# Kernel optimization log

Hardware: AMD Instinct MI355X
Metric: run time of the kernel (lower is better)

## Reference

```python
import jax, jax.numpy as jnp
import numpy as np

FEATS = 1024
HEAD = 16
MLP_HIDDEN = 4096
HEAD_DIM = FEATS // HEAD
SQRT_D = float(FEATS) ** 0.5  # module scales by sqrt(feats), not sqrt(head_dim)
LN_EPS = 1e-5


def layer_norm(x, g, b):
    mu = jnp.mean(x, axis=-1, keepdims=True)
    var = jnp.mean(jnp.square(x - mu), axis=-1, keepdims=True)
    return (x - mu) * jax.lax.rsqrt(var + LN_EPS) * g + b


def setup_inputs() -> dict:
    key = jax.random.key(0)
    ks = jax.random.split(key, 12)
    s = 1.0 / np.sqrt(FEATS)
    s2 = 1.0 / np.sqrt(MLP_HIDDEN)
    return {
        "x": jax.random.normal(ks[0], (2, 2048, FEATS), dtype=jnp.float32),
        "ln1_g": jnp.ones((FEATS,), jnp.float32),
        "ln1_b": jnp.zeros((FEATS,), jnp.float32),
        "wq": jax.random.normal(ks[1], (FEATS, FEATS), jnp.float32) * s,
        "bq": jnp.zeros((FEATS,), jnp.float32),
        "wk": jax.random.normal(ks[2], (FEATS, FEATS), jnp.float32) * s,
        "bk": jnp.zeros((FEATS,), jnp.float32),
        "wv": jax.random.normal(ks[3], (FEATS, FEATS), jnp.float32) * s,
        "bv": jnp.zeros((FEATS,), jnp.float32),
        "wo": jax.random.normal(ks[4], (FEATS, FEATS), jnp.float32) * s,
        "bo": jnp.zeros((FEATS,), jnp.float32),
        "ln2_g": jnp.ones((FEATS,), jnp.float32),
        "ln2_b": jnp.zeros((FEATS,), jnp.float32),
        "w1": jax.random.normal(ks[5], (MLP_HIDDEN, FEATS), jnp.float32) * s,
        "b1": jnp.zeros((MLP_HIDDEN,), jnp.float32),
        "w2": jax.random.normal(ks[6], (FEATS, MLP_HIDDEN), jnp.float32) * s2,
        "b2": jnp.zeros((FEATS,), jnp.float32),
    }


def reference(x, ln1_g, ln1_b, wq, bq, wk, bk, wv, bv, wo, bo,
              ln2_g, ln2_b, w1, b1, w2, b2):
    b, n, f = x.shape
    h = layer_norm(x, ln1_g, ln1_b)
    # qkv projections (torch Linear: y = x @ W.T + b)
    q = (h @ wq.T + bq).reshape(b, n, HEAD, HEAD_DIM).transpose(0, 2, 1, 3)
    k = (h @ wk.T + bk).reshape(b, n, HEAD, HEAD_DIM).transpose(0, 2, 1, 3)
    v = (h @ wv.T + bv).reshape(b, n, HEAD, HEAD_DIM).transpose(0, 2, 1, 3)
    score = jax.nn.softmax(jnp.einsum('bhif,bhjf->bhij', q, k) / SQRT_D, axis=-1)
    attn = jnp.einsum('bhij,bhjf->bihf', score, v).reshape(b, n, f)
    o = attn @ wo.T + bo
    out1 = o + x
    h2 = layer_norm(out1, ln2_g, ln2_b)
    mlp = jax.nn.relu(jax.nn.relu(h2 @ w1.T + b1) @ w2.T + b2)
    return mlp + out1
```

## Files before the change

kernel.cpp:

```cpp
#include <hip/hip_runtime.h>
#include <hip/hip_bf16.h>

#define FEATS 1024
#define NH 16
#define HD 64
#define SEQ 2048
#define BATCH 2
#define MTOT (BATCH*SEQ)
#define MLPH 4096
#define QSCALE 0.04508422277369218f

typedef __attribute__((ext_vector_type(8))) short bf16x8;
typedef __attribute__((ext_vector_type(4))) short bf16x4;
typedef __attribute__((ext_vector_type(4))) float f32x4;

static_assert(sizeof(bf16x8) == 16, "bf16x8 must be 16B");

__device__ __forceinline__ unsigned short f2bf(float f) {
    unsigned int u = __float_as_uint(f);
    unsigned int lsb = (u >> 16) & 1u;
    u += 0x7fffu + lsb;
    return (unsigned short)(u >> 16);
}

#define ASYNC16(GP, LP) __builtin_amdgcn_global_load_lds( \
    (const __attribute__((address_space(1))) void*)(GP),  \
    (__attribute__((address_space(3))) void*)(LP), 16, 0, 0)

__global__ __launch_bounds__(256) void cvt_all_kernel(
    const float* __restrict__ wq, const float* __restrict__ wk,
    const float* __restrict__ wv, const float* __restrict__ wo,
    const float* __restrict__ w1, const float* __restrict__ w2,
    unsigned short* __restrict__ dst) {
    const size_t i = ((size_t)blockIdx.x * 256 + threadIdx.x) * 4;
    const size_t MB = (size_t)1024 * 1024;
    const float* s;
    size_t off;
    float sc = 1.0f;
    if (i < MB)            { s = wq; off = i;          sc = QSCALE; }
    else if (i < 2 * MB)   { s = wk; off = i - MB; }
    else if (i < 3 * MB)   { s = wv; off = i - 2 * MB; }
    else if (i < 4 * MB)   { s = wo; off = i - 3 * MB; }
    else if (i < 8 * MB)   { s = w1; off = i - 4 * MB; }
    else                   { s = w2; off = i - 8 * MB; }
    float4 v = *(const float4*)(s + off);
    ushort4 o;
    o.x = f2bf(v.x * sc); o.y = f2bf(v.y * sc);
    o.z = f2bf(v.z * sc); o.w = f2bf(v.w * sc);
    *(ushort4*)(dst + i) = o;
}

__global__ __launch_bounds__(256) void concat3_kernel(const float* __restrict__ a,
                                                      const float* __restrict__ b,
                                                      const float* __restrict__ c,
                                                      float* __restrict__ o) {
    int i = blockIdx.x * 256 + threadIdx.x;
    float v = (i < 1024) ? a[i] * QSCALE : ((i < 2048) ? b[i - 1024] : c[i - 2048]);
    o[i] = v;
}

__global__ __launch_bounds__(256) void ln_kernel(const float* __restrict__ x,
                                                 const float* __restrict__ g,
                                                 const float* __restrict__ bta,
                                                 unsigned short* __restrict__ h) {
    __shared__ float red[8];
    const int row = blockIdx.x;
    const int t = threadIdx.x;
    const float* xr = x + (size_t)row * FEATS;
    float4 v = ((const float4*)xr)[t];
    float s  = v.x + v.y + v.z + v.w;
    float ss = v.x * v.x + v.y * v.y + v.z * v.z + v.w * v.w;
#pragma unroll
    for (int off = 1; off < 64; off <<= 1) {
        s  += __shfl_xor(s, off);
        ss += __shfl_xor(ss, off);
    }
    const int w = t >> 6;
    if ((t & 63) == 0) { red[w] = s; red[4 + w] = ss; }
    __syncthreads();
    s  = red[0] + red[1] + red[2] + red[3];
    ss = red[4] + red[5] + red[6] + red[7];
    const float mu  = s * (1.f / FEATS);
    const float var = ss * (1.f / FEATS) - mu * mu;
    const float rs  = rsqrtf(var + 1e-5f);
    float4 gv = ((const float4*)g)[t];
    float4 bv = ((const float4*)bta)[t];
    ushort4 ov;
    ov.x = f2bf((v.x - mu) * rs * gv.x + bv.x);
    ov.y = f2bf((v.y - mu) * rs * gv.y + bv.y);
    ov.z = f2bf((v.z - mu) * rs * gv.z + bv.z);
    ov.w = f2bf((v.w - mu) * rs * gv.w + bv.w);
    ((ushort4*)h)[(size_t)row * (FEATS / 4) + t] = ov;
}

template <bool RELU, bool ADD, bool OUTBF16>
__global__ __launch_bounds__(256, 3)
void gemm_kernel(const unsigned short* __restrict__ A,
                 const unsigned short* __restrict__ W,
                 const float* __restrict__ bias,
                 const float* __restrict__ addend,
                 void* __restrict__ outp,
                 int M, int N, int K, int gx) {
    __shared__ unsigned short lds[3][2][128 * 32];

    const int t = threadIdx.x;
    const int w = t >> 6, lane = t & 63;
    const int wr = w >> 1, wc = w & 1;
    const int li = lane & 15, lj = lane >> 4;

    const int nwg = gridDim.x;
    const int cpx = nwg >> 3;
    const int wg = blockIdx.x;
    const int swz = (wg & 7) * cpx + (wg >> 3);
    const int mb = (swz / gx) * 128, nb = (swz % gx) * 128;

    const int srow = lane >> 2;
    const int scg = ((lane & 3) ^ (srow & 3)) * 8;
    const unsigned short* gA = A + (size_t)(mb + w * 16 + srow) * K + scg;
    const unsigned short* gB = W + (size_t)(nb + w * 16 + srow) * K + scg;
    const size_t half = (size_t)64 * K;
    const int lbase = w * 512 + lane * 8;

    const int rsw = (lj ^ (li & 3)) * 8;

    const int nt = K >> 5;

#define STAGE(BUF, K0)                                             \
    do {                                                           \
        unsigned short* la_ = &lds[BUF][0][lbase];                 \
        unsigned short* lb_ = &lds[BUF][1][lbase];                 \
        ASYNC16(gA + (K0), la_);                                   \
        ASYNC16(gA + half + (K0), la_ + 2048);                     \
        ASYNC16(gB + (K0), lb_);                                   \
        ASYNC16(gB + half + (K0), lb_ + 2048);                     \
    } while (0)

    STAGE(0, 0);
    STAGE(1, 32);
    asm volatile("s_waitcnt vmcnt(4)" ::: "memory");
    __builtin_amdgcn_s_barrier();

    f32x4 acc[4][4] = {};

    for (int i = 0; i < nt; ++i) {
        const int cur = i % 3;
        const unsigned short* Al = &lds[cur][0][0];
        const unsigned short* Bl = &lds[cur][1][0];

        bf16x8 af[4], bfr[4];
#pragma unroll
        for (int m = 0; m < 4; m++)
            af[m] = *(const bf16x8*)(Al + (wr * 64 + m * 16 + li) * 32 + rsw);
#pragma unroll
        for (int n = 0; n < 4; n++)
            bfr[n] = *(const bf16x8*)(Bl + (wc * 64 + n * 16 + li) * 32 + rsw);

        const int pf = i + 2 < nt;
        if (pf) STAGE((i + 2) % 3, (i + 2) * 32);

#pragma unroll
        for (int m = 0; m < 4; m++)
#pragma unroll
            for (int n = 0; n < 4; n++)
                acc[m][n] = __builtin_amdgcn_mfma_f32_16x16x32_bf16(af[m], bfr[n], acc[m][n], 0, 0, 0);

        if (i + 1 < nt) {
            if (pf) asm volatile("s_waitcnt vmcnt(4)" ::: "memory");
            else    asm volatile("s_waitcnt vmcnt(0)" ::: "memory");
            __builtin_amdgcn_s_barrier();
        }
    }
#undef STAGE

#pragma unroll
    for (int m = 0; m < 4; m++) {
#pragma unroll
        for (int n = 0; n < 4; n++) {
            const int col = nb + wc * 64 + n * 16 + li;
            const float bv = bias[col];
#pragma unroll
            for (int r = 0; r < 4; r++) {
                const int row = mb + wr * 64 + m * 16 + lj * 4 + r;
                float v = acc[m][n][r] + bv;
                if (RELU) v = fmaxf(v, 0.f);
                if (ADD)  v += addend[(size_t)row * N + col];
                if (OUTBF16)
                    ((unsigned short*)outp)[(size_t)row * N + col] = f2bf(v);
                else
                    ((float*)outp)[(size_t)row * N + col] = v;
            }
        }
    }
}

__global__ __launch_bounds__(256) void vtrans_kernel(const unsigned short* __restrict__ qkv,
                                                     unsigned short* __restrict__ vt) {
    constexpr int LDV = 68;
    __shared__ unsigned short Vl[64 * LDV];
    const int bh = blockIdx.x, st = blockIdx.y;
    const int b = bh >> 4, h = bh & 15;
    const int t = threadIdx.x;
    const unsigned short* src = qkv + (size_t)(b * SEQ + st * 64) * (3 * FEATS) + 2 * FEATS + h * HD;
#pragma unroll
    for (int i = 0; i < 2; i++) {
        int idx = t + i * 256;
        int r = idx >> 3, c = (idx & 7) * 8;
        *(bf16x8*)(Vl + r * LDV + c) = *(const bf16x8*)(src + (size_t)r * (3 * FEATS) + c);
    }
    __syncthreads();
    unsigned short* dst = vt + (size_t)bh * HD * SEQ + st * 64;
#pragma unroll
    for (int i = 0; i < 2; i++) {
        int idx = t + i * 256;
        int d = idx >> 3, s8 = (idx & 7) * 8;
        bf16x8 v;
#pragma unroll
        for (int j = 0; j < 8; j++) v[j] = Vl[(s8 + j) * LDV + d];
        *(bf16x8*)(dst + (size_t)d * SEQ + s8) = v;
    }
}

__global__ __launch_bounds__(256, 2)
void attn_kernel(const unsigned short* __restrict__ qkv,
                 const unsigned short* __restrict__ vt,
                 unsigned short* __restrict__ out) {
    constexpr int LK = 72;
    constexpr int LV = 136;
    __shared__ unsigned short Kl[2][128 * LK];
    __shared__ unsigned short Vtl[2][64 * LV];

    const int bh = blockIdx.x;
    const int b = bh >> 4, h = bh & 15;
    const int q0 = blockIdx.y * 128;
    const int t = threadIdx.x, w = t >> 6, lane = t & 63;
    const int li = lane & 15, lj = lane >> 4;

    const size_t rstr = 3 * FEATS;
    const unsigned short* qkvb = qkv + (size_t)(b * SEQ) * rstr;
    const unsigned short* ksrc = qkvb + FEATS + h * HD;
    const unsigned short* vsrc = vt + (size_t)bh * HD * SEQ;

    bf16x8 aq[2][2];
#pragma unroll
    for (int hh = 0; hh < 2; hh++)
#pragma unroll
        for (int kk = 0; kk < 2; kk++)
            aq[hh][kk] = *(const bf16x8*)(qkvb +
                (size_t)(q0 + w * 32 + hh * 16 + li) * rstr + h * HD + kk * 32 + lj * 8);

    f32x4 o[2][4] = {};
    f32x4 oS[2] = {};

    const short onebf = (short)0x3F80;
    const bf16x8 ones = {onebf, onebf, onebf, onebf, onebf, onebf, onebf, onebf};

    const int skey = t >> 1, dbase = (t & 1) * 32;
    const unsigned short* kg = ksrc + (size_t)skey * rstr + dbase;
    const int ldoK = skey * LK + dbase;
    const int sd = t >> 2, kbase = (t & 3) * 32;
    const unsigned short* vg = vsrc + (size_t)sd * SEQ + kbase;
    const int ldoV = sd * LV + kbase;

    const int nt = SEQ / 128;

#define KW(BUF, R0, R1, R2, R3)                          \
    do {                                                 \
        *(bf16x8*)(&Kl[BUF][ldoK])      = R0;            \
        *(bf16x8*)(&Kl[BUF][ldoK + 8])  = R1;            \
        *(bf16x8*)(&Kl[BUF][ldoK + 16]) = R2;            \
        *(bf16x8*)(&Kl[BUF][ldoK + 24]) = R3;            \
    } while (0)
#define VW1(BUF, VR, POS)                                                              \
    do {                                                                               \
        *(bf16x4*)(&Vtl[BUF][(POS)])     = __builtin_shufflevector(VR, VR, 0, 1, 2, 3);\
        *(bf16x4*)(&Vtl[BUF][(POS) + 8]) = __builtin_shufflevector(VR, VR, 4, 5, 6, 7);\
    } while (0)
#define VW(BUF, V0, V1, V2, V3)                          \
    do {                                                 \
        VW1(BUF, V0, ldoV);                              \
        VW1(BUF, V1, ldoV + 16);                         \
        VW1(BUF, V2, ldoV + 4);                          \
        VW1(BUF, V3, ldoV + 20);                         \
    } while (0)

    {
        bf16x8 k0 = *(const bf16x8*)kg;
        bf16x8 k1 = *(const bf16x8*)(kg + 8);
        bf16x8 k2 = *(const bf16x8*)(kg + 16);
        bf16x8 k3 = *(const bf16x8*)(kg + 24);
        bf16x8 v0 = *(const bf16x8*)vg;
        bf16x8 v1 = *(const bf16x8*)(vg + 8);
        bf16x8 v2 = *(const bf16x8*)(vg + 16);
        bf16x8 v3 = *(const bf16x8*)(vg + 24);
        KW(0, k0, k1, k2, k3);
        VW(0, v0, v1, v2, v3);
    }

    int cur = 0;
    for (int i = 0; i < nt; ++i) {
        bf16x8 kr0, kr1, kr2, kr3, vr0, vr1, vr2, vr3;
        if (i + 1 < nt) {
            const unsigned short* kn = kg + (size_t)(i + 1) * 128 * rstr;
            const unsigned short* vn = vg + (i + 1) * 128;
            kr0 = *(const bf16x8*)kn;
            kr1 = *(const bf16x8*)(kn + 8);
            kr2 = *(const bf16x8*)(kn + 16);
            kr3 = *(const bf16x8*)(kn + 24);
            vr0 = *(const bf16x8*)vn;
            vr1 = *(const bf16x8*)(vn + 8);
            vr2 = *(const bf16x8*)(vn + 16);
            vr3 = *(const bf16x8*)(vn + 24);
        }

        asm volatile("s_waitcnt lgkmcnt(0)" ::: "memory");
        __builtin_amdgcn_s_barrier();

        const unsigned short* Kc = Kl[cur];
        const unsigned short* Vc = Vtl[cur];

        f32x4 s[2][8];
        __builtin_amdgcn_s_setprio(1);
#pragma unroll
        for (int n = 0; n < 8; n++) {
            bf16x8 k0 = *(const bf16x8*)(Kc + (n * 16 + li) * LK + lj * 8);
            bf16x8 k1 = *(const bf16x8*)(Kc + (n * 16 + li) * LK + 32 + lj * 8);
#pragma unroll
            for (int hh = 0; hh < 2; hh++) {
                f32x4 acc = {};
                acc = __builtin_amdgcn_mfma_f32_16x16x32_bf16(k0, aq[hh][0], acc, 0, 0, 0);
                acc = __builtin_amdgcn_mfma_f32_16x16x32_bf16(k1, aq[hh][1], acc, 0, 0, 0);
                s[hh][n] = acc;
            }
        }
        __builtin_amdgcn_s_setprio(0);

        bf16x8 A[2][4];
#pragma unroll
        for (int hh = 0; hh < 2; hh++)
#pragma unroll
            for (int kk = 0; kk < 4; kk++) {
                float p[8];
#pragma unroll
                for (int r = 0; r < 4; r++) {
                    p[r]     = exp2f(s[hh][2 * kk][r]);
                    p[4 + r] = exp2f(s[hh][2 * kk + 1][r]);
                }
                union { unsigned u[4]; bf16x8 v; } Au;
                asm("v_cvt_pk_bf16_f32 %0, %1, %2" : "=v"(Au.u[0]) : "v"(p[0]), "v"(p[1]));
                asm("v_cvt_pk_bf16_f32 %0, %1, %2" : "=v"(Au.u[1]) : "v"(p[2]), "v"(p[3]));
                asm("v_cvt_pk_bf16_f32 %0, %1, %2" : "=v"(Au.u[2]) : "v"(p[4]), "v"(p[5]));
                asm("v_cvt_pk_bf16_f32 %0, %1, %2" : "=v"(Au.u[3]) : "v"(p[6]), "v"(p[7]));
                A[hh][kk] = Au.v;
            }

#pragma unroll
        for (int hh = 0; hh < 2; hh++)
#pragma unroll
            for (int kk = 0; kk < 4; kk++)
                oS[hh] = __builtin_amdgcn_mfma_f32_16x16x32_bf16(A[hh][kk], ones, oS[hh], 0, 0, 0);

        __builtin_amdgcn_s_setprio(1);
#pragma unroll
        for (int n = 0; n < 4; n++) {
#pragma unroll
            for (int kk = 0; kk < 4; kk++) {
                bf16x8 bv = *(const bf16x8*)(Vc + (n * 16 + li) * LV + kk * 32 + lj * 8);
                o[0][n] = __builtin_amdgcn_mfma_f32_16x16x32_bf16(A[0][kk], bv, o[0][n], 0, 0, 0);
                o[1][n] = __builtin_amdgcn_mfma_f32_16x16x32_bf16(A[1][kk], bv, o[1][n], 0, 0, 0);
            }
        }
        __builtin_amdgcn_s_setprio(0);

        if (i + 1 < nt) {
            KW(cur ^ 1, kr0, kr1, kr2, kr3);
            VW(cur ^ 1, vr0, vr1, vr2, vr3);
        }
        cur ^= 1;
    }
#undef KW
#undef VW
#undef VW1

    unsigned short* ob = out + (size_t)(b * SEQ + q0 + w * 32) * FEATS + h * HD;
#pragma unroll
    for (int hh = 0; hh < 2; hh++)
#pragma unroll
        for (int r = 0; r < 4; r++) {
            const float inv = 1.f / oS[hh][r];
#pragma unroll
            for (int n = 0; n < 4; n++)
                ob[(size_t)(hh * 16 + lj * 4 + r) * FEATS + n * 16 + li] =
                    f2bf(o[hh][n][r] * inv);
        }
}

extern "C" void kernel_launch(void* const* d_in, const int* in_sizes, int n_in,
                              void* d_out, int out_size, void* d_ws, size_t ws_size,
                              hipStream_t stream) {
    const float* x     = (const float*)d_in[0];
    const float* ln1_g = (const float*)d_in[1];
    const float* ln1_b = (const float*)d_in[2];
    const float* wq    = (const float*)d_in[3];
    const float* bq    = (const float*)d_in[4];
    const float* wk    = (const float*)d_in[5];
    const float* bk    = (const float*)d_in[6];
    const float* wv    = (const float*)d_in[7];
    const float* bvv   = (const float*)d_in[8];
    const float* wo    = (const float*)d_in[9];
    const float* bo    = (const float*)d_in[10];
    const float* ln2_g = (const float*)d_in[11];
    const float* ln2_b = (const float*)d_in[12];
    const float* w1    = (const float*)d_in[13];
    const float* b1    = (const float*)d_in[14];
    const float* w2    = (const float*)d_in[15];
    const float* b2    = (const float*)d_in[16];

    unsigned short* wqkv_b = (unsigned short*)d_ws;
    unsigned short* wo_b   = wqkv_b + 3072 * 1024;
    unsigned short* w1_b   = wo_b + 1024 * 1024;
    unsigned short* w2_b   = w1_b + 4096 * 1024;
    float*          bqkv   = (float*)(w2_b + 1024 * 4096);
    unsigned short* region = (unsigned short*)(bqkv + 3072);
    unsigned short* qkvb   = region;
    unsigned short* hb     = region + (size_t)4096 * 3072;
    unsigned short* vtb    = hb;
    unsigned short* a1     = region;
    unsigned short* attn_o = region + (size_t)4096 * 4096;
    unsigned short* h2     = attn_o;
    float*          out1   = (float*)(attn_o + (size_t)4096 * 1024);
    float*          outf   = (float*)d_out;

    dim3 blk(256);

    cvt_all_kernel<<<12288, blk, 0, stream>>>(wq, wk, wv, wo, w1, w2, wqkv_b);
    concat3_kernel<<<12, blk, 0, stream>>>(bq, bk, bvv, bqkv);

    ln_kernel<<<MTOT, blk, 0, stream>>>(x, ln1_g, ln1_b, hb);

    gemm_kernel<false, false, true><<<768, blk, 0, stream>>>(
        hb, wqkv_b, bqkv, nullptr, qkvb, MTOT, 3072, FEATS, 24);

    vtrans_kernel<<<dim3(BATCH * NH, SEQ / 64), blk, 0, stream>>>(qkvb, vtb);

    attn_kernel<<<dim3(BATCH * NH, SEQ / 128), dim3(256), 0, stream>>>(qkvb, vtb, attn_o);

    gemm_kernel<false, true, false><<<256, blk, 0, stream>>>(
        attn_o, wo_b, bo, x, out1, MTOT, FEATS, FEATS, 8);

    ln_kernel<<<MTOT, blk, 0, stream>>>(out1, ln2_g, ln2_b, h2);

    gemm_kernel<true, false, true><<<1024, blk, 0, stream>>>(
        h2, w1_b, b1, nullptr, a1, MTOT, MLPH, FEATS, 32);

    gemm_kernel<true, true, false><<<256, blk, 0, stream>>>(
        a1, w2_b, b2, out1, outf, MTOT, FEATS, MLPH, 8);
}
```

Before: 232.7 us.

## Load K and V fragments directly from global memory, dropping LDS staging

```diff
diff --git a/kernel.cpp b/kernel.cpp
--- a/kernel.cpp
+++ b/kernel.cpp
@@ -213,22 +213,22 @@
     for (int i = 0; i < 2; i++) {
         int idx = t + i * 256;
         int d = idx >> 3, s8 = (idx & 7) * 8;
+        const int base = s8 & ~31;
+        const int u4 = ((s8 >> 3) & 3) * 4;
         bf16x8 v;
 #pragma unroll
-        for (int j = 0; j < 8; j++) v[j] = Vl[(s8 + j) * LDV + d];
+        for (int j = 0; j < 8; j++) {
+            const int key = base + u4 + (j & 3) + ((j >> 2) & 1) * 16;
+            v[j] = Vl[key * LDV + d];
+        }
         *(bf16x8*)(dst + (size_t)d * SEQ + s8) = v;
     }
 }
 
-__global__ __launch_bounds__(256, 2)
+__global__ __launch_bounds__(256, 3)
 void attn_kernel(const unsigned short* __restrict__ qkv,
                  const unsigned short* __restrict__ vt,
                  unsigned short* __restrict__ out) {
-    constexpr int LK = 72;
-    constexpr int LV = 136;
-    __shared__ unsigned short Kl[2][128 * LK];
-    __shared__ unsigned short Vtl[2][64 * LV];
-
     const int bh = blockIdx.x;
     const int b = bh >> 4, h = bh & 15;
     const int q0 = blockIdx.y * 128;
@@ -237,8 +237,6 @@
 
     const size_t rstr = 3 * FEATS;
     const unsigned short* qkvb = qkv + (size_t)(b * SEQ) * rstr;
-    const unsigned short* ksrc = qkvb + FEATS + h * HD;
-    const unsigned short* vsrc = vt + (size_t)bh * HD * SEQ;
 
     bf16x8 aq[2][2];
 #pragma unroll
@@ -254,76 +252,21 @@
     const short onebf = (short)0x3F80;
     const bf16x8 ones = {onebf, onebf, onebf, onebf, onebf, onebf, onebf, onebf};
 
-    const int skey = t >> 1, dbase = (t & 1) * 32;
-    const unsigned short* kg = ksrc + (size_t)skey * rstr + dbase;
-    const int ldoK = skey * LK + dbase;
-    const int sd = t >> 2, kbase = (t & 3) * 32;
-    const unsigned short* vg = vsrc + (size_t)sd * SEQ + kbase;
-    const int ldoV = sd * LV + kbase;
-
-    const int nt = SEQ / 128;
-
-#define KW(BUF, R0, R1, R2, R3)                          \
-    do {                                                 \
-        *(bf16x8*)(&Kl[BUF][ldoK])      = R0;            \
-        *(bf16x8*)(&Kl[BUF][ldoK + 8])  = R1;            \
-        *(bf16x8*)(&Kl[BUF][ldoK + 16]) = R2;            \
-        *(bf16x8*)(&Kl[BUF][ldoK + 24]) = R3;            \
-    } while (0)
-#define VW1(BUF, VR, POS)                                                              \
-    do {                                                                               \
-        *(bf16x4*)(&Vtl[BUF][(POS)])     = __builtin_shufflevector(VR, VR, 0, 1, 2, 3);\
-        *(bf16x4*)(&Vtl[BUF][(POS) + 8]) = __builtin_shufflevector(VR, VR, 4, 5, 6, 7);\
-    } while (0)
-#define VW(BUF, V0, V1, V2, V3)                          \
-    do {                                                 \
-        VW1(BUF, V0, ldoV);                              \
-        VW1(BUF, V1, ldoV + 16);                         \
-        VW1(BUF, V2, ldoV + 4);                          \
-        VW1(BUF, V3, ldoV + 20);                         \
-    } while (0)
-
-    {
-        bf16x8 k0 = *(const bf16x8*)kg;
-        bf16x8 k1 = *(const bf16x8*)(kg + 8);
-        bf16x8 k2 = *(const bf16x8*)(kg + 16);
-        bf16x8 k3 = *(const bf16x8*)(kg + 24);
-        bf16x8 v0 = *(const bf16x8*)vg;
-        bf16x8 v1 = *(const bf16x8*)(vg + 8);
-        bf16x8 v2 = *(const bf16x8*)(vg + 16);
-        bf16x8 v3 = *(const bf16x8*)(vg + 24);
-        KW(0, k0, k1, k2, k3);
-        VW(0, v0, v1, v2, v3);
-    }
-
-    int cur = 0;
-    for (int i = 0; i < nt; ++i) {
-        bf16x8 kr0, kr1, kr2, kr3, vr0, vr1, vr2, vr3;
-        if (i + 1 < nt) {
-            const unsigned short* kn = kg + (size_t)(i + 1) * 128 * rstr;
-            const unsigned short* vn = vg + (i + 1) * 128;
-            kr0 = *(const bf16x8*)kn;
-            kr1 = *(const bf16x8*)(kn + 8);
-            kr2 = *(const bf16x8*)(kn + 16);
-            kr3 = *(const bf16x8*)(kn + 24);
-            vr0 = *(const bf16x8*)vn;
-            vr1 = *(const bf16x8*)(vn + 8);
-            vr2 = *(const bf16x8*)(vn + 16);
-            vr3 = *(const bf16x8*)(vn + 24);
-        }
-
-        asm volatile("s_waitcnt lgkmcnt(0)" ::: "memory");
-        __builtin_amdgcn_s_barrier();
-
-        const unsigned short* Kc = Kl[cur];
-        const unsigned short* Vc = Vtl[cur];
-
-        f32x4 s[2][8];
+    const unsigned short* krow[4];
+    const unsigned short* vrow[4];
+#pragma unroll
+    for (int n = 0; n < 4; n++) {
+        krow[n] = qkvb + FEATS + h * HD + (size_t)(n * 16 + li) * rstr + lj * 8;
+        vrow[n] = vt + (size_t)bh * HD * SEQ + (size_t)(n * 16 + li) * SEQ + lj * 8;
+    }
+
+    for (int kv0 = 0; kv0 < SEQ; kv0 += 64) {
+        f32x4 s[2][4];
         __builtin_amdgcn_s_setprio(1);
 #pragma unroll
-        for (int n = 0; n < 8; n++) {
-            bf16x8 k0 = *(const bf16x8*)(Kc + (n * 16 + li) * LK + lj * 8);
-            bf16x8 k1 = *(const bf16x8*)(Kc + (n * 16 + li) * LK + 32 + lj * 8);
+        for (int n = 0; n < 4; n++) {
+            bf16x8 k0 = *(const bf16x8*)(krow[n]);
+            bf16x8 k1 = *(const bf16x8*)(krow[n] + 32);
 #pragma unroll
             for (int hh = 0; hh < 2; hh++) {
                 f32x4 acc = {};
@@ -334,11 +277,18 @@
         }
         __builtin_amdgcn_s_setprio(0);
 
-        bf16x8 A[2][4];
+        bf16x8 vf[4][2];
+#pragma unroll
+        for (int n = 0; n < 4; n++)
+#pragma unroll
+            for (int kk = 0; kk < 2; kk++)
+                vf[n][kk] = *(const bf16x8*)(vrow[n] + kk * 32);
+
+        bf16x8 A[2][2];
 #pragma unroll
         for (int hh = 0; hh < 2; hh++)
 #pragma unroll
-            for (int kk = 0; kk < 4; kk++) {
+            for (int kk = 0; kk < 2; kk++) {
                 float p[8];
 #pragma unroll
                 for (int r = 0; r < 4; r++) {
@@ -356,30 +306,25 @@
 #pragma unroll
         for (int hh = 0; hh < 2; hh++)
 #pragma unroll
-            for (int kk = 0; kk < 4; kk++)
+            for (int kk = 0; kk < 2; kk++)
                 oS[hh] = __builtin_amdgcn_mfma_f32_16x16x32_bf16(A[hh][kk], ones, oS[hh], 0, 0, 0);
 
         __builtin_amdgcn_s_setprio(1);
 #pragma unroll
+        for (int n = 0; n < 4; n++)
+#pragma unroll
+            for (int kk = 0; kk < 2; kk++) {
+                o[0][n] = __builtin_amdgcn_mfma_f32_16x16x32_bf16(A[0][kk], vf[n][kk], o[0][n], 0, 0, 0);
+                o[1][n] = __builtin_amdgcn_mfma_f32_16x16x32_bf16(A[1][kk], vf[n][kk], o[1][n], 0, 0, 0);
+            }
+        __builtin_amdgcn_s_setprio(0);
+
+#pragma unroll
         for (int n = 0; n < 4; n++) {
-#pragma unroll
-            for (int kk = 0; kk < 4; kk++) {
-                bf16x8 bv = *(const bf16x8*)(Vc + (n * 16 + li) * LV + kk * 32 + lj * 8);
-                o[0][n] = __builtin_amdgcn_mfma_f32_16x16x32_bf16(A[0][kk], bv, o[0][n], 0, 0, 0);
-                o[1][n] = __builtin_amdgcn_mfma_f32_16x16x32_bf16(A[1][kk], bv, o[1][n], 0, 0, 0);
-            }
-        }
-        __builtin_amdgcn_s_setprio(0);
-
-        if (i + 1 < nt) {
-            KW(cur ^ 1, kr0, kr1, kr2, kr3);
-            VW(cur ^ 1, vr0, vr1, vr2, vr3);
-        }
-        cur ^= 1;
-    }
-#undef KW
-#undef VW
-#undef VW1
+            krow[n] += (size_t)64 * rstr;
+            vrow[n] += 64;
+        }
+    }
 
     unsigned short* ob = out + (size_t)(b * SEQ + q0 + w * 32) * FEATS + h * HD;
 #pragma unroll
```

Result: slower. 296.0 us (+27.2%).
